# Optimization experiments

Measured on AMD Instinct MI355X. Metric: run time of the kernel, lower is better.

The kernel has to match this reference:

```python
import jax, jax.numpy as jnp
import numpy as np

BETA = 4.0  # temperature of soft cluster assignment in filling loss


def _pairwise_sq_dist(a, b):
    # a: [N,D], b: [K,D] -> [N,K] squared euclidean distances
    return (jnp.sum(a * a, -1, keepdims=True)
            - 2.0 * (a @ b.T)
            + jnp.sum(b * b, -1)[None, :])


def setup_inputs() -> dict:
    key = jax.random.key(0)
    k1, k2, k3, k4 = jax.random.split(key, 4)
    N, D, K = 131072, 64, 16
    x = jax.random.normal(k1, (N, D), jnp.float32)
    cluster_centers = jax.random.normal(k2, (K, D), jnp.float32)
    target = jax.random.normal(k3, (N, D), jnp.float32)
    ft = jax.random.uniform(k4, (K,), jnp.float32)
    filling_target = ft / ft.sum()
    # prediction = kmeans assignment of the fixed target set (computed once, constant)
    prediction = jnp.argmin(_pairwise_sq_dist(target, cluster_centers), axis=-1)
    return {"x": x, "cluster_centers": cluster_centers,
            "filling_target": filling_target, "target": target,
            "prediction": prediction}


def reference(x, cluster_centers, filling_target, target, prediction):
    N, D = x.shape
    Nt = target.shape[0]
    K = cluster_centers.shape[0]
    BIG = jnp.finfo(x.dtype).max  # padding value that sorts to the end

    d2 = _pairwise_sq_dist(x, cluster_centers)  # [N,K]

    # --- cluster filling MSE: soft assignment fractions vs filling_target ---
    soft = jax.nn.softmax(-BETA * d2, axis=-1)          # [N,K]
    filling = soft.mean(axis=0)                          # [K]
    loss_fil = jnp.mean((filling - filling_target) ** 2)

    # --- per-cluster sorted (per-dimension 1D) Wasserstein distance ---
    pred_x = jax.lax.stop_gradient(jnp.argmin(d2, axis=-1))  # kmeans_predict(x).detach()
    L = min(N, Nt)  # static upper bound on per-cluster min_size
    rows = jnp.arange(L)

    loss_med = jnp.zeros((), x.dtype)
    for k in range(K):  # fixed structural loop over clusters
        mx = pred_x == k
        mt = prediction == k
        m = jnp.minimum(mx.sum(), mt.sum())  # min_size (dynamic value, static shapes)
        # keep only the FIRST m members (original order), as x[in_cluster][:m]
        keep_x = mx & ((jnp.cumsum(mx) - 1) < m)
        keep_t = mt & ((jnp.cumsum(mt) - 1) < m)
        # mask out non-members with BIG so they sort to the bottom, sort per dim
        xs = jnp.sort(jnp.where(keep_x[:, None], x, BIG), axis=0)[:L]       # [L,D]
        ts = jnp.sort(jnp.where(keep_t[:, None], target, BIG), axis=0)[:L]  # [L,D]
        valid = (rows < m)[:, None]                                          # [L,1]
        diff = jnp.where(valid, jnp.abs(xs - ts), 0.0)
        # mean(|sort(x) - sort(y)|) over the m x D selected elements
        denom = (m * D).astype(x.dtype)
        loss_med = loss_med + jnp.where(m > 0, diff.sum() / denom, 0.0)

    return loss_fil + loss_med
```

## Files before the change

### kernel.cpp

```cpp
#include <hip/hip_runtime.h>
#include <stdint.h>

#define N_ROWS 131072
#define DIMS 64
#define KCL 16
#define BETA 4.0f
#define NBLK 512
#define CHUNK 16384
#define STH 1024
#define SEG_STRIDE 263168
#define VOFF (1u<<21)

typedef unsigned long long u64;
typedef unsigned int u32;

__device__ __forceinline__ u32 enc_f(float f) {
  u32 u = __float_as_uint(f);
  return (u & 0x80000000u) ? ~u : (u | 0x80000000u);
}
__device__ __forceinline__ float dec_f(u32 e) {
  u32 u = (e & 0x80000000u) ? (e & 0x7FFFFFFFu) : ~e;
  return __uint_as_float(u);
}
__device__ __forceinline__ u32 U4(u32 u) { return u ^ ((u >> 3) & 7u); }

#define CS(a,b,dd) { u32 _mn = min(a,b), _mx = max(a,b); a = (dd)?_mn:_mx; b = (dd)?_mx:_mn; }
#define CSV(A,B,D) { CS(A.x,B.x,D) CS(A.y,B.y,D) CS(A.z,B.z,D) CS(A.w,B.w,D) }

#define M16G(a,b,c,d,e,f,g,h,i2,j2,k2,l,m,n,o,p,D) \
  CS(a,i2,D) CS(b,j2,D) CS(c,k2,D) CS(d,l,D) CS(e,m,D) CS(f,n,D) CS(g,o,D) CS(h,p,D) \
  CS(a,e,D)  CS(b,f,D)  CS(c,g,D)  CS(d,h,D) CS(i2,m,D) CS(j2,n,D) CS(k2,o,D) CS(l,p,D) \
  CS(a,c,D)  CS(b,d,D)  CS(e,g,D)  CS(f,h,D) CS(i2,k2,D) CS(j2,l,D) CS(m,o,D) CS(n,p,D) \
  CS(a,b,D)  CS(c,d,D)  CS(e,f,D)  CS(g,h,D) CS(i2,j2,D) CS(k2,l,D) CS(m,n,D) CS(o,p,D)

#define SORT16G(a,b,c,d,e,f,g,h,i2,j2,k2,l,m,n,o,p,D) \
  CS(a,b,D) CS(c,d,!(D)) CS(e,f,D) CS(g,h,!(D)) CS(i2,j2,D) CS(k2,l,!(D)) CS(m,n,D) CS(o,p,!(D)) \
  CS(a,c,D) CS(b,d,D) CS(e,g,!(D)) CS(f,h,!(D)) CS(i2,k2,D) CS(j2,l,D) CS(m,o,!(D)) CS(n,p,!(D)) \
  CS(a,b,D) CS(c,d,D) CS(e,f,!(D)) CS(g,h,!(D)) CS(i2,j2,D) CS(k2,l,D) CS(m,n,!(D)) CS(o,p,!(D)) \
  CS(a,e,D) CS(b,f,D) CS(c,g,D) CS(d,h,D) CS(i2,m,!(D)) CS(j2,n,!(D)) CS(k2,o,!(D)) CS(l,p,!(D)) \
  CS(a,c,D) CS(b,d,D) CS(e,g,D) CS(f,h,D) CS(i2,k2,!(D)) CS(j2,l,!(D)) CS(m,o,!(D)) CS(n,p,!(D)) \
  CS(a,b,D) CS(c,d,D) CS(e,f,D) CS(g,h,D) CS(i2,j2,!(D)) CS(k2,l,!(D)) CS(m,n,!(D)) CS(o,p,!(D)) \
  M16G(a,b,c,d,e,f,g,h,i2,j2,k2,l,m,n,o,p,D)

#define MERGE16F(D) M16G(r0,r1,r2,r3,r4,r5,r6,r7,r8,r9,r10,r11,r12,r13,r14,r15,D)
#define SORT16F(D)  SORT16G(r0,r1,r2,r3,r4,r5,r6,r7,r8,r9,r10,r11,r12,r13,r14,r15,D)

#define LOADTILE16(src) \
  { uint4 _a0=src[U4(ub+0)],_a1=src[U4(ub+1)],_a2=src[U4(ub+2)],_a3=src[U4(ub+3)]; \
    r0=_a0.x;r1=_a0.y;r2=_a0.z;r3=_a0.w; r4=_a1.x;r5=_a1.y;r6=_a1.z;r7=_a1.w; \
    r8=_a2.x;r9=_a2.y;r10=_a2.z;r11=_a2.w; r12=_a3.x;r13=_a3.y;r14=_a3.z;r15=_a3.w; }

#define STORETILE16(dst) \
  { dst[U4(ub+0)]=make_uint4(r0,r1,r2,r3);   dst[U4(ub+1)]=make_uint4(r4,r5,r6,r7); \
    dst[U4(ub+2)]=make_uint4(r8,r9,r10,r11); dst[U4(ub+3)]=make_uint4(r12,r13,r14,r15); }

__device__ __forceinline__ void wave_tail(uint4* lds4, u32 RU, u32 Lw, u32 gbase,
                                          u32 k, u32 jtop, u32 lane)
{
  u32 j = jtop;
  while (j >= 32u) {
    u32 ud = j >> 3;
    if (lane < (Lw >> 4)) {
      u32 bu = RU + (((lane & ~(ud - 1u)) << 2) | (lane & (ud - 1u)));
      bool up = (((gbase + (bu << 2)) & k) == 0u);
      uint4 A0 = lds4[U4(bu)],           A1 = lds4[U4(bu + ud)],
            A2 = lds4[U4(bu + 2u * ud)], A3 = lds4[U4(bu + 3u * ud)];
      CSV(A0,A2,up) CSV(A1,A3,up)
      CSV(A0,A1,up) CSV(A2,A3,up)
      lds4[U4(bu)] = A0;           lds4[U4(bu + ud)] = A1;
      lds4[U4(bu + 2u * ud)] = A2; lds4[U4(bu + 3u * ud)] = A3;
    }
    j >>= 2;
  }
  if (j == 16u) {
    u32 total = Lw >> 3;
    for (u32 inst = lane; inst < total; inst += 64u) {
      u32 bu = RU + (((inst & ~3u) << 1) | (inst & 3u));
      bool up = (((gbase + (bu << 2)) & k) == 0u);
      uint4 A = lds4[U4(bu)], B = lds4[U4(bu + 4u)];
      CSV(A,B,up)
      lds4[U4(bu)] = A; lds4[U4(bu + 4u)] = B;
    }
  }
}

__device__ __forceinline__ void cross1(uint4* lds4, u32 Wn, u32 gb, u32 k, u32 jtop, u32 tid)
{
  u32 ud = jtop >> 2;
  u32 total = Wn >> 3;
  for (u32 inst = tid; inst < total; inst += STH) {
    u32 bu = ((inst & ~(ud - 1u)) << 1) | (inst & (ud - 1u));
    bool up = (((gb + (bu << 2)) & k) == 0u);
    uint4 A = lds4[U4(bu)], B = lds4[U4(bu + ud)];
    CSV(A,B,up)
    lds4[U4(bu)] = A; lds4[U4(bu + ud)] = B;
  }
}
__device__ __forceinline__ void cross2(uint4* lds4, u32 Wn, u32 gb, u32 k, u32 jtop, u32 tid)
{
  u32 ud = jtop >> 3;
  u32 total = Wn >> 4;
  for (u32 inst = tid; inst < total; inst += STH) {
    u32 bu = ((inst & ~(ud - 1u)) << 2) | (inst & (ud - 1u));
    bool up = (((gb + (bu << 2)) & k) == 0u);
    uint4 A0 = lds4[U4(bu)],            A1 = lds4[U4(bu + ud)],
          A2 = lds4[U4(bu + 2u * ud)],  A3 = lds4[U4(bu + 3u * ud)];
    CSV(A0,A2,up) CSV(A1,A3,up)
    CSV(A0,A1,up) CSV(A2,A3,up)
    lds4[U4(bu)] = A0;           lds4[U4(bu + ud)] = A1;
    lds4[U4(bu + 2u * ud)] = A2; lds4[U4(bu + 3u * ud)] = A3;
  }
}
__device__ __forceinline__ void cross3(uint4* lds4, u32 Wn, u32 gb, u32 k, u32 jtop, u32 tid)
{
  u32 ud = jtop >> 4;
  u32 total = Wn >> 5;
  for (u32 inst = tid; inst < total; inst += STH) {
    u32 bu = ((inst & ~(ud - 1u)) << 3) | (inst & (ud - 1u));
    bool up = (((gb + (bu << 2)) & k) == 0u);
    uint4 A0 = lds4[U4(bu)],            A1 = lds4[U4(bu + ud)],
          A2 = lds4[U4(bu + 2u * ud)],  A3 = lds4[U4(bu + 3u * ud)],
          A4 = lds4[U4(bu + 4u * ud)],  A5 = lds4[U4(bu + 5u * ud)],
          A6 = lds4[U4(bu + 6u * ud)],  A7 = lds4[U4(bu + 7u * ud)];
    CSV(A0,A4,up) CSV(A1,A5,up) CSV(A2,A6,up) CSV(A3,A7,up)
    CSV(A0,A2,up) CSV(A1,A3,up) CSV(A4,A6,up) CSV(A5,A7,up)
    CSV(A0,A1,up) CSV(A2,A3,up) CSV(A4,A5,up) CSV(A6,A7,up)
    lds4[U4(bu)] = A0;           lds4[U4(bu + ud)] = A1;
    lds4[U4(bu + 2u * ud)] = A2; lds4[U4(bu + 3u * ud)] = A3;
    lds4[U4(bu + 4u * ud)] = A4; lds4[U4(bu + 5u * ud)] = A5;
    lds4[U4(bu + 6u * ud)] = A6; lds4[U4(bu + 7u * ud)] = A7;
  }
}

__global__ __launch_bounds__(256) void k_assign(
    const float* __restrict__ x, const float* __restrict__ centers,
    const int* __restrict__ predT, int* __restrict__ predX,
    float* __restrict__ fill_sum, u32* __restrict__ histX, u32* __restrict__ histT)
{
  __shared__ float c[KCL][DIMS];
  __shared__ float cn[KCL];
  __shared__ float fs[KCL];
  __shared__ u32 hx[KCL], ht[KCL];
  int tid = threadIdx.x;
  for (int t = tid; t < KCL * DIMS; t += 256) c[t / DIMS][t % DIMS] = centers[t];
  if (tid < KCL) { fs[tid] = 0.f; hx[tid] = 0; ht[tid] = 0; }
  __syncthreads();
  if (tid < KCL) {
    float s = 0.f;
    for (int d = 0; d < DIMS; ++d) s += c[tid][d] * c[tid][d];
    cn[tid] = s;
  }
  __syncthreads();
  int i = blockIdx.x * 256 + tid;
  const float4* xr = (const float4*)(x + (size_t)i * DIMS);
  float dot[KCL];
#pragma unroll
  for (int k = 0; k < KCL; ++k) dot[k] = 0.f;
  for (int t = 0; t < DIMS / 4; ++t) {
    float4 v = xr[t];
#pragma unroll
    for (int k = 0; k < KCL; ++k)
      dot[k] += v.x * c[k][4 * t] + v.y * c[k][4 * t + 1] + v.z * c[k][4 * t + 2] + v.w * c[k][4 * t + 3];
  }
  float sc[KCL];
  float smin = 3.0e38f; int kmin = 0;
#pragma unroll
  for (int k = 0; k < KCL; ++k) {
    sc[k] = cn[k] - 2.f * dot[k];
    if (sc[k] < smin) { smin = sc[k]; kmin = k; }
  }
  float e[KCL]; float esum = 0.f;
#pragma unroll
  for (int k = 0; k < KCL; ++k) { e[k] = expf(-BETA * (sc[k] - smin)); esum += e[k]; }
  float inv = 1.f / esum;
#pragma unroll
  for (int k = 0; k < KCL; ++k) atomicAdd(&fs[k], e[k] * inv);
  predX[i] = kmin;
  atomicAdd(&hx[kmin], 1u);
  atomicAdd(&ht[predT[i]], 1u);
  __syncthreads();
  if (tid < KCL) {
    histX[blockIdx.x * KCL + tid] = hx[tid];
    histT[blockIdx.x * KCL + tid] = ht[tid];
    atomicAdd(&fill_sum[tid], fs[tid]);
  }
}

__global__ __launch_bounds__(512) void k_scan(
    const u32* __restrict__ histX, const u32* __restrict__ histT,
    u32* __restrict__ baseX, u32* __restrict__ baseT,
    const float* __restrict__ fill_sum, const float* __restrict__ ftarget,
    int* __restrict__ m_out, float* __restrict__ w_out,
    int* __restrict__ p_out, int* __restrict__ pOff_out, int* __restrict__ mOff_out,
    int* __restrict__ nlo_out, float* __restrict__ loss_fil)
{
  __shared__ u32 part[2][KCL][17];
  __shared__ u32 tot[2][KCL];
  __shared__ float sq[KCL];
  __shared__ int sp[KCL];
  __shared__ int smv[KCL];
  int tid = threadIdx.x;
  int side = tid >> 8;
  int rem = tid & 255;
  int c = rem >> 4;
  int sub = rem & 15;
  const u32* hist = side ? histT : histX;
  u32* base = side ? baseT : baseX;
  int b0 = sub * 32;
  u32 s = 0;
  for (int b = b0; b < b0 + 32; ++b) s += hist[b * KCL + c];
  part[side][c][sub] = s;
  __syncthreads();
  if (sub == 0) {
    u32 run = 0;
    for (int t = 0; t < 16; ++t) { u32 v = part[side][c][t]; part[side][c][t] = run; run += v; }
    tot[side][c] = run;
  }
  __syncthreads();
  u32 run = part[side][c][sub];
  for (int b = b0; b < b0 + 32; ++b) { base[b * KCL + c] = run; run += hist[b * KCL + c]; }
  if (tid < KCL) {
    int m = min((int)tot[0][tid], (int)tot[1][tid]);
    m_out[tid] = m;
    smv[tid] = m;
    w_out[tid] = (m > 0) ? 1.f / ((float)m * (float)DIMS) : 0.f;
    int pp = 32;
    while (pp < m) pp <<= 1;
    sp[tid] = pp;
    p_out[tid] = pp;
    int nlo = 0;
    if (pp > CHUNK) {
      int nch = pp / CHUNK;
      for (int j = 1; j < nch; j += 2) {
        int v = m - j * CHUNK;
        if (v < 0) v = 0;
        if (v > CHUNK) v = CHUNK;
        nlo += CHUNK - v;
      }
    }
    nlo_out[tid] = nlo;
    float d = fill_sum[tid] / (float)N_ROWS - ftarget[tid];
    sq[tid] = d * d;
  }
  __syncthreads();
  if (tid == 0) {
    float s2 = 0.f;
    int acc = 0, macc = 0;
    for (int k = 0; k < KCL; ++k) {
      s2 += sq[k];
      pOff_out[k] = acc;
      acc += sp[k];
      mOff_out[k] = macc;
      macc += smv[k];
    }
    pOff_out[KCL] = acc;
    mOff_out[KCL] = macc;
    *loss_fil = s2 / (float)KCL;
  }
}

__global__ __launch_bounds__(256) void k_rank(
    const int* __restrict__ predX, const int* __restrict__ predT,
    const u32* __restrict__ baseX, const u32* __restrict__ baseT,
    const int* __restrict__ mG, const int* __restrict__ mOffG,
    int* __restrict__ idxX, int* __restrict__ idxT)
{
  __shared__ int wcX[4][KCL], wcT[4][KCL];
  __shared__ int smo[KCL], sm2[KCL];
  int tid = threadIdx.x;
  int lane = tid & 63, wave = tid >> 6;
  if (tid < KCL) { smo[tid] = mOffG[tid]; sm2[tid] = mG[tid]; }
  int i = blockIdx.x * 256 + tid;
  int kx = predX[i], kt = predT[i];
  u64 below = (1ull << lane) - 1ull;
  int lrX = 0, lrT = 0;
  for (int cc = 0; cc < KCL; ++cc) {
    u64 mx = __ballot(kx == cc);
    u64 mt = __ballot(kt == cc);
    if (kx == cc) lrX = __popcll(mx & below);
    if (kt == cc) lrT = __popcll(mt & below);
    if (lane == 0) { wcX[wave][cc] = __popcll(mx); wcT[wave][cc] = __popcll(mt); }
  }
  __syncthreads();
  int wbX = 0, wbT = 0;
  for (int w2 = 0; w2 < wave; ++w2) { wbX += wcX[w2][kx]; wbT += wcT[w2][kt]; }
  int rX = (int)baseX[blockIdx.x * KCL + kx] + wbX + lrX;
  int rT = (int)baseT[blockIdx.x * KCL + kt] + wbT + lrT;
  if (rX < sm2[kx]) idxX[smo[kx] + rX] = i;
  if (rT < sm2[kt]) idxT[smo[kt] + rT] = i;
}

__global__ __launch_bounds__(256) void k_gather(
    const float* __restrict__ x, const float* __restrict__ tgt,
    const int* __restrict__ idxX, const int* __restrict__ idxT,
    const int* __restrict__ pOffG, const int* __restrict__ mOffG,
    const int* __restrict__ mG, const int* __restrict__ pG,
    u32* __restrict__ valX, u32* __restrict__ valT, int d0, int Dbc)
{
  __shared__ int spOff[KCL + 1];
  __shared__ int smo[KCL], sm2[KCL], sp2[KCL];
  __shared__ float pl[32][257];
  __shared__ int sRowX[256], sRowT[256];
  __shared__ u32 sPv[256];
  int tid = threadIdx.x;
  if (tid <= KCL) spOff[tid] = pOffG[tid];
  if (tid < KCL) { smo[tid] = mOffG[tid]; sm2[tid] = mG[tid]; sp2[tid] = pG[tid]; }
  __syncthreads();
  int pos = blockIdx.x * 256 + tid;
  bool inr = pos < spOff[KCL];
  int c = 0, rel = 0;
  bool vld = false;
  if (inr) {
#pragma unroll
    for (int cc = 1; cc < KCL; ++cc) c += (pos >= spOff[cc]) ? 1 : 0;
    rel = pos - spOff[c];
    vld = rel < sm2[c];
  }

  if (Dbc == 64) {
    int w = vld ? (smo[c] + rel) : 0;
    sRowX[tid] = vld ? idxX[w] : -1;
    sRowT[tid] = vld ? idxT[w] : -1;
    sPv[tid] = inr ? ((sp2[c] > CHUNK && ((rel >> 14) & 1)) ? 0u : 0xFFFFFFFFu) : 0u;
    __syncthreads();
#pragma unroll
    for (int side = 0; side < 2; ++side) {
      const float* src = side ? tgt : x;
      const int* sRow = side ? sRowT : sRowX;
      u32* dst = side ? valT : valX;
#pragma unroll
      for (int h = 0; h < 2; ++h) {
        int h0 = h * 32;
        for (int idx = tid; idx < 256 * 8; idx += 256) {
          int r = idx >> 3, f = idx & 7;
          int row = sRow[r];
          if (row >= 0) {
            float4 v = *(const float4*)(src + (size_t)row * DIMS + d0 + h0 + f * 4);
            pl[f * 4 + 0][r] = v.x;
            pl[f * 4 + 1][r] = v.y;
            pl[f * 4 + 2][r] = v.z;
            pl[f * 4 + 3][r] = v.w;
          }
        }
        __syncthreads();
        if (inr) {
          bool v2 = sRow[tid] >= 0;
          u32 pv = sPv[tid];
          for (int dl = 0; dl < 32; ++dl) {
            u32 e = v2 ? enc_f(pl[dl][tid]) : pv;
            dst[(size_t)(h0 + dl) * SEG_STRIDE + pos] = e;
          }
        }
        __syncthreads();
      }
    }
    return;
  }

  if (!inr) return;
  u32* dx = valX + pos;
  u32* dt = valT + pos;
  if (vld) {
    int w = smo[c] + rel;
    int iX = idxX[w], iT = idxT[w];
    const float* xr = x + (size_t)iX * DIMS + d0;
    const float* tr = tgt + (size_t)iT * DIMS + d0;
    for (int d = 0; d < Dbc; ++d) {
      dx[(size_t)d * SEG_STRIDE] = enc_f(xr[d]);
      dt[(size_t)d * SEG_STRIDE] = enc_f(tr[d]);
    }
  } else {
    u32 pv = (sp2[c] > CHUNK && ((rel >> 14) & 1)) ? 0u : 0xFFFFFFFFu;
    for (int d = 0; d < Dbc; ++d) {
      dx[(size_t)d * SEG_STRIDE] = pv;
      dt[(size_t)d * SEG_STRIDE] = pv;
    }
  }
}

__global__ __launch_bounds__(STH, 8) void k_sort(
    u32* __restrict__ vbase, const int* __restrict__ pG, const int* __restrict__ pOffG,
    const int* __restrict__ mG)
{
  __shared__ __align__(16) u32 lds[CHUNK];
  uint4* lds4 = (uint4*)lds;
  int t = blockIdx.x, c = -1, sub = 0, acc = 0;
  for (int cc = 0; cc < KCL; ++cc) {
    int pc0 = pG[cc];
    int nc = (pc0 > CHUNK) ? (pc0 / CHUNK) : 1;
    if (t < acc + nc) { c = cc; sub = t - acc; break; }
    acc += nc;
  }
  if (c < 0) return;
  int pc = pG[c];
  u32 CH = (u32)min(pc, CHUNK);
  u32 gb = (u32)sub * (u32)CHUNK;
  int v = mG[c] - (int)gb;
  if (v > (int)CH) v = (int)CH;
  if (v <= 0) return;
  u32 W = 32u;
  while (W < (u32)v) W <<= 1;
  if (W > CH) W = CH;
  bool desc = (pc > CHUNK) && (sub & 1);
  u32 inv = desc ? 0xFFFFFFFFu : 0u;
  u32* seg = vbase + (size_t)blockIdx.y * SEG_STRIDE + pOffG[c] + gb;
  uint4* gp4 = (uint4*)seg;
  u32 tid = threadIdx.x;
  u32 lane = tid & 63u;
  u32 wv = tid >> 6;
  u32 ub = tid << 2;
  u32 bas = tid << 4;
  bool act = (bas < W);
  u32 RU = wv << 8;
  u32 runBase = wv << 10;
  bool wact = (runBase < W);
  u32 Lw = W - runBase; if (Lw > 1024u) Lw = 1024u;
  u32 r0,r1,r2,r3,r4,r5,r6,r7,r8,r9,r10,r11,r12,r13,r14,r15;

  if (act) {
    uint4 a0 = gp4[ub + 0], a1 = gp4[ub + 1], a2 = gp4[ub + 2], a3 = gp4[ub + 3];
    r0 = a0.x^inv; r1 = a0.y^inv; r2  = a0.z^inv; r3  = a0.w^inv;
    r4 = a1.x^inv; r5 = a1.y^inv; r6  = a1.z^inv; r7  = a1.w^inv;
    r8 = a2.x^inv; r9 = a2.y^inv; r10 = a2.z^inv; r11 = a2.w^inv;
    r12 = a3.x^inv; r13 = a3.y^inv; r14 = a3.z^inv; r15 = a3.w^inv;
    bool D = ((bas & 16u) == 0u);
    SORT16F(D);
    STORETILE16(lds4);
  }
  if (wact) {
    for (u32 k = 32u; k <= Lw; k <<= 1) {
      wave_tail(lds4, RU, Lw, 0u, k, k >> 1, lane);
      if (act) {
        LOADTILE16(lds4);
        bool D = ((bas & k) == 0u);
        MERGE16F(D);
        STORETILE16(lds4);
      }
    }
  }

  if (W >= 2048u) {
    __syncthreads();
    for (u32 k = 2048u; k <= W; k <<= 1) {
      u32 jt = k >> 1;
      if (jt >= 8192u) {
        cross3(lds4, W, 0u, k, 8192u, tid);
        __syncthreads();
        cross1(lds4, W, 0u, k, 1024u, tid);
        __syncthreads();
      } else if (jt == 4096u) {
        cross3(lds4, W, 0u, k, 4096u, tid);
        __syncthreads();
      } else if (jt == 2048u) {
        cross2(lds4, W, 0u, k, 2048u, tid);
        __syncthreads();
      } else {
        cross1(lds4, W, 0u, k, 1024u, tid);
        __syncthreads();
      }
      if (wact) {
        wave_tail(lds4, RU, Lw, 0u, k, 512u, lane);
        if (act) {
          LOADTILE16(lds4);
          bool D = ((bas & k) == 0u);
          MERGE16F(D);
          STORETILE16(lds4);
        }
      }
      if (k < W) __syncthreads();
    }
  }

  __syncthreads();
  for (u32 uu = tid; (uu << 2) < W; uu += STH) {
    uint4 q = lds4[U4(uu)];
    q.x ^= inv; q.y ^= inv; q.z ^= inv; q.w ^= inv;
    gp4[uu] = q;
  }
}

__global__ __launch_bounds__(256) void k_gpass(
    u32* __restrict__ vbase, const int* __restrict__ pG, const int* __restrict__ pOffG,
    int kk, int j)
{
  u32* base = vbase + (size_t)blockIdx.y * SEG_STRIDE;
  int pb[KCL]; int tot = 0;
#pragma unroll
  for (int c = 0; c < KCL; ++c) {
    pb[c] = tot;
    int pc = pG[c];
    if (pc >= kk) tot += pc >> 1;
  }
  for (int g4 = (blockIdx.x * 256 + threadIdx.x) << 2; g4 < tot; g4 += gridDim.x * 256 * 4) {
    int c = 0;
#pragma unroll
    for (int cc = 1; cc < KCL; ++cc) c += (g4 >= pb[cc]) ? 1 : 0;
    int u = g4 - pb[c];
    int i = ((u & ~(j - 1)) << 1) | (u & (j - 1));
    bool up = ((i & kk) == 0);
    u32* s2 = base + pOffG[c];
    uint4 A = *(const uint4*)(s2 + i);
    uint4 B = *(const uint4*)(s2 + i + j);
    CS(A.x, B.x, up) CS(A.y, B.y, up) CS(A.z, B.z, up) CS(A.w, B.w, up)
    *(uint4*)(s2 + i) = A;
    *(uint4*)(s2 + i + j) = B;
  }
}

__global__ __launch_bounds__(STH) void k_gfinish(
    u32* __restrict__ vbase, const int* __restrict__ pG, const int* __restrict__ pOffG, int kk)
{
  __shared__ __align__(16) u32 lds[CHUNK];
  uint4* lds4 = (uint4*)lds;
  int t = blockIdx.x, c = -1, sub = 0, acc = 0;
  for (int cc = 0; cc < KCL; ++cc) {
    int pc = pG[cc];
    if (pc < kk) continue;
    int nc = pc / CHUNK;
    if (t < acc + nc) { c = cc; sub = t - acc; break; }
    acc += nc;
  }
  if (c < 0) return;
  u32 gb = (u32)sub * (u32)CHUNK;
  u32* seg = vbase + (size_t)blockIdx.y * SEG_STRIDE + pOffG[c] + gb;
  uint4* gp4 = (uint4*)seg;
  u32 tid = threadIdx.x;
  u32 lane = tid & 63u;
  u32 wv = tid >> 6;
  u32 RU = wv << 8;
  u32 ub = tid << 2;
  u32 bas = tid << 4;
  u32 r0,r1,r2,r3,r4,r5,r6,r7,r8,r9,r10,r11,r12,r13,r14,r15;

  for (u32 uu = tid; uu < CHUNK / 4; uu += STH) lds4[U4(uu)] = gp4[uu];
  __syncthreads();
  cross3(lds4, (u32)CHUNK, gb, (u32)kk, 8192u, tid);
  __syncthreads();
  cross1(lds4, (u32)CHUNK, gb, (u32)kk, 1024u, tid);
  __syncthreads();
  wave_tail(lds4, RU, 1024u, gb, (u32)kk, 512u, lane);
  {
    LOADTILE16(lds4);
    bool up = (((gb + bas) & (u32)kk) == 0u);
    MERGE16F(up);
    STORETILE16(lds4);
  }
  __syncthreads();
  for (u32 uu = tid; uu < CHUNK / 4; uu += STH) gp4[uu] = lds4[U4(uu)];
}

__global__ __launch_bounds__(256) void k_reduce(
    const u32* __restrict__ valX, const u32* __restrict__ valT,
    const int* __restrict__ pOffG, const int* __restrict__ mOffG,
    const int* __restrict__ nloG,
    const float* __restrict__ wG, float* __restrict__ lossAcc)
{
  __shared__ int spOff[KCL];
  __shared__ int smo[KCL + 1];
  __shared__ int snlo[KCL];
  __shared__ float swt[KCL];
  __shared__ float red[256];
  int tid = threadIdx.x;
  if (tid <= KCL) smo[tid] = mOffG[tid];
  if (tid < KCL) { spOff[tid] = pOffG[tid]; snlo[tid] = nloG[tid]; swt[tid] = wG[tid]; }
  __syncthreads();
  int d = blockIdx.y;
  const u32* vx = valX + (size_t)d * SEG_STRIDE;
  const u32* vt = valT + (size_t)d * SEG_STRIDE;
  int M = smo[KCL];
  float s = 0.f;
  for (int w = blockIdx.x * 256 + tid; w < M; w += gridDim.x * 256) {
    int c = 0;
#pragma unroll
    for (int cc = 1; cc < KCL; ++cc) c += (w >= smo[cc]) ? 1 : 0;
    int pos = spOff[c] + snlo[c] + (w - smo[c]);
    float a = dec_f(vx[pos]), b = dec_f(vt[pos]);
    s += fabsf(a - b) * swt[c];
  }
  red[tid] = s;
  __syncthreads();
  for (int st = 128; st > 0; st >>= 1) {
    if (tid < st) red[tid] += red[tid + st];
    __syncthreads();
  }
  if (tid == 0) atomicAdd(lossAcc, red[0]);
}

__global__ void k_final(const float* __restrict__ lossAcc, const float* __restrict__ loss_fil,
                        float* __restrict__ out)
{
  out[0] = *lossAcc + *loss_fil;
}

extern "C" void kernel_launch(void* const* d_in, const int* in_sizes, int n_in,
                              void* d_out, int out_size, void* d_ws, size_t ws_size,
                              hipStream_t stream)
{
  const float* x       = (const float*)d_in[0];
  const float* centers = (const float*)d_in[1];
  const float* ftarget = (const float*)d_in[2];
  const float* tgt     = (const float*)d_in[3];
  const int*   predT   = (const int*)d_in[4];
  float* out = (float*)d_out;

  char* ws = (char*)d_ws;
  float* fill_sum = (float*)(ws + 0);
  float* lossAcc  = (float*)(ws + 64);
  float* loss_fil = (float*)(ws + 68);
  int*   m_buf    = (int*)(ws + 128);
  float* w_buf    = (float*)(ws + 192);
  int*   p_buf    = (int*)(ws + 256);
  int*   pOff     = (int*)(ws + 320);
  int*   mOff     = (int*)(ws + 400);
  u32* histX = (u32*)(ws + 512);
  u32* histT = (u32*)(ws + 512 + 32768);
  u32* baseX = (u32*)(ws + 512 + 65536);
  u32* baseT = (u32*)(ws + 512 + 98304);
  int* predX = (int*)(ws + 131584);
  int* idxX  = (int*)(ws + 655872);
  int* idxT  = (int*)(ws + 1180160);
  int* nlo_buf = (int*)(ws + 1704448);
  u32* vbase = (u32*)(ws + VOFF);

  size_t avail_elems = (ws_size > VOFF) ? ((ws_size - VOFF) / 4) : 0;
  int Db = (int)(avail_elems / (2ull * SEG_STRIDE));
  if (Db > DIMS) Db = DIMS;
  if (Db >= 4) Db &= ~3;
  if (Db < 1) Db = 1;

  hipMemsetAsync(ws, 0, 128, stream);
  k_assign<<<NBLK, 256, 0, stream>>>(x, centers, predT, predX, fill_sum, histX, histT);
  k_scan<<<1, 512, 0, stream>>>(histX, histT, baseX, baseT, fill_sum, ftarget,
                                m_buf, w_buf, p_buf, pOff, mOff, nlo_buf, loss_fil);
  k_rank<<<NBLK, 256, 0, stream>>>(predX, predT, baseX, baseT, m_buf, mOff, idxX, idxT);

  for (int d0 = 0; d0 < DIMS; d0 += Db) {
    int Dbc = (Db < DIMS - d0) ? Db : (DIMS - d0);
    u32* valX = vbase;
    u32* valT = vbase + (size_t)Dbc * SEG_STRIDE;
    k_gather<<<1028, 256, 0, stream>>>(x, tgt, idxX, idxT, pOff, mOff, m_buf, p_buf,
                                       valX, valT, d0, Dbc);
    k_sort<<<dim3(28, 2 * Dbc), STH, 0, stream>>>(vbase, p_buf, pOff, m_buf);
    for (int kk = 2 * CHUNK; kk <= N_ROWS; kk <<= 1) {
      int gx = (kk == 2 * CHUNK) ? 32 : 8;
      for (int j = kk >> 1; j >= CHUNK; j >>= 1)
        k_gpass<<<dim3(gx, 2 * Dbc), 256, 0, stream>>>(vbase, p_buf, pOff, kk, j);
      k_gfinish<<<dim3(18, 2 * Dbc), STH, 0, stream>>>(vbase, p_buf, pOff, kk);
    }
    k_reduce<<<dim3(32, Dbc), 256, 0, stream>>>(valX, valT, pOff, mOff, nlo_buf,
                                                w_buf, lossAcc);
  }
  k_final<<<1, 1, 0, stream>>>(lossAcc, loss_fil, out);
}
```

Baseline: 599.3 us.

## Fuse small-cluster loss reduction into target sort kernel

The per-dimension sort is split into an X sort kernel and a T sort kernel. For clusters that fit in one chunk, the T sort kernel reads the already sorted X values and accumulates the weighted absolute difference directly, so those sorted T values are never written back to global memory. The separate reduce kernel now covers only the large multi-chunk clusters with fewer blocks. This saves a global write and re-read for small clusters, but it serialises the two sorts into back-to-back launches with half the blocks each, and it depends on the X sort finishing before the T sort reads its output.

```diff
diff --git a/kernel.cpp b/kernel.cpp
--- a/kernel.cpp
+++ b/kernel.cpp
@@ -378,7 +378,7 @@
   }
 }
 
-__global__ __launch_bounds__(STH, 8) void k_sort(
+__global__ __launch_bounds__(STH, 8) void k_sortX(
     u32* __restrict__ vbase, const int* __restrict__ pG, const int* __restrict__ pOffG,
     const int* __restrict__ mG)
 {
@@ -479,6 +479,149 @@
   }
 }
 
+__global__ __launch_bounds__(STH, 8) void k_sortT(
+    u32* __restrict__ vbase, const int* __restrict__ pG, const int* __restrict__ pOffG,
+    const int* __restrict__ mG, const float* __restrict__ wG,
+    float* __restrict__ lossAcc, int Dbc)
+{
+  __shared__ __align__(16) u32 lds[CHUNK];
+  uint4* lds4 = (uint4*)lds;
+  int t = blockIdx.x, c = -1, sub = 0, acc = 0;
+  for (int cc = 0; cc < KCL; ++cc) {
+    int pc0 = pG[cc];
+    int nc = (pc0 > CHUNK) ? (pc0 / CHUNK) : 1;
+    if (t < acc + nc) { c = cc; sub = t - acc; break; }
+    acc += nc;
+  }
+  if (c < 0) return;
+  int pc = pG[c];
+  u32 CH = (u32)min(pc, CHUNK);
+  u32 gb = (u32)sub * (u32)CHUNK;
+  int v = mG[c] - (int)gb;
+  if (v > (int)CH) v = (int)CH;
+  if (v <= 0) return;
+  u32 W = 32u;
+  while (W < (u32)v) W <<= 1;
+  if (W > CH) W = CH;
+  bool big = (pc > CHUNK);
+  bool desc = big && (sub & 1);
+  u32 inv = desc ? 0xFFFFFFFFu : 0u;
+  u32* segX = vbase + (size_t)blockIdx.y * SEG_STRIDE + pOffG[c] + gb;
+  u32* segT = segX + (size_t)Dbc * SEG_STRIDE;
+  uint4* gp4 = (uint4*)segT;
+  const uint4* gpX4 = (const uint4*)segX;
+  u32 tid = threadIdx.x;
+  u32 lane = tid & 63u;
+  u32 wv = tid >> 6;
+  u32 ub = tid << 2;
+  u32 bas = tid << 4;
+  bool act = (bas < W);
+  u32 RU = wv << 8;
+  u32 runBase = wv << 10;
+  bool wact = (runBase < W);
+  u32 Lw = W - runBase; if (Lw > 1024u) Lw = 1024u;
+  u32 r0,r1,r2,r3,r4,r5,r6,r7,r8,r9,r10,r11,r12,r13,r14,r15;
+
+  if (act) {
+    uint4 a0 = gp4[ub + 0], a1 = gp4[ub + 1], a2 = gp4[ub + 2], a3 = gp4[ub + 3];
+    r0 = a0.x^inv; r1 = a0.y^inv; r2  = a0.z^inv; r3  = a0.w^inv;
+    r4 = a1.x^inv; r5 = a1.y^inv; r6  = a1.z^inv; r7  = a1.w^inv;
+    r8 = a2.x^inv; r9 = a2.y^inv; r10 = a2.z^inv; r11 = a2.w^inv;
+    r12 = a3.x^inv; r13 = a3.y^inv; r14 = a3.z^inv; r15 = a3.w^inv;
+    bool D = ((bas & 16u) == 0u);
+    SORT16F(D);
+    STORETILE16(lds4);
+  }
+  if (wact) {
+    for (u32 k = 32u; k <= Lw; k <<= 1) {
+      wave_tail(lds4, RU, Lw, 0u, k, k >> 1, lane);
+      if (act) {
+        LOADTILE16(lds4);
+        bool D = ((bas & k) == 0u);
+        MERGE16F(D);
+        STORETILE16(lds4);
+      }
+    }
+  }
+
+  if (W >= 2048u) {
+    __syncthreads();
+    for (u32 k = 2048u; k <= W; k <<= 1) {
+      u32 jt = k >> 1;
+      if (jt >= 8192u) {
+        cross3(lds4, W, 0u, k, 8192u, tid);
+        __syncthreads();
+        cross1(lds4, W, 0u, k, 1024u, tid);
+        __syncthreads();
+      } else if (jt == 4096u) {
+        cross3(lds4, W, 0u, k, 4096u, tid);
+        __syncthreads();
+      } else if (jt == 2048u) {
+        cross2(lds4, W, 0u, k, 2048u, tid);
+        __syncthreads();
+      } else {
+        cross1(lds4, W, 0u, k, 1024u, tid);
+        __syncthreads();
+      }
+      if (wact) {
+        wave_tail(lds4, RU, Lw, 0u, k, 512u, lane);
+        if (act) {
+          LOADTILE16(lds4);
+          bool D = ((bas & k) == 0u);
+          MERGE16F(D);
+          STORETILE16(lds4);
+        }
+      }
+      if (k < W) __syncthreads();
+    }
+  }
+  __syncthreads();
+
+  if (big) {
+    for (u32 uu = tid; (uu << 2) < W; uu += STH) {
+      uint4 q = lds4[U4(uu)];
+      q.x ^= inv; q.y ^= inv; q.z ^= inv; q.w ^= inv;
+      gp4[uu] = q;
+    }
+    return;
+  }
+
+  float s = 0.f;
+  if (act) {
+    LOADTILE16(lds4);
+    uint4 b0 = gpX4[ub + 0], b1 = gpX4[ub + 1], b2 = gpX4[ub + 2], b3 = gpX4[ub + 3];
+    u32 vv = (u32)v;
+    if (bas + 0u  < vv) s += fabsf(dec_f(b0.x) - dec_f(r0));
+    if (bas + 1u  < vv) s += fabsf(dec_f(b0.y) - dec_f(r1));
+    if (bas + 2u  < vv) s += fabsf(dec_f(b0.z) - dec_f(r2));
+    if (bas + 3u  < vv) s += fabsf(dec_f(b0.w) - dec_f(r3));
+    if (bas + 4u  < vv) s += fabsf(dec_f(b1.x) - dec_f(r4));
+    if (bas + 5u  < vv) s += fabsf(dec_f(b1.y) - dec_f(r5));
+    if (bas + 6u  < vv) s += fabsf(dec_f(b1.z) - dec_f(r6));
+    if (bas + 7u  < vv) s += fabsf(dec_f(b1.w) - dec_f(r7));
+    if (bas + 8u  < vv) s += fabsf(dec_f(b2.x) - dec_f(r8));
+    if (bas + 9u  < vv) s += fabsf(dec_f(b2.y) - dec_f(r9));
+    if (bas + 10u < vv) s += fabsf(dec_f(b2.z) - dec_f(r10));
+    if (bas + 11u < vv) s += fabsf(dec_f(b2.w) - dec_f(r11));
+    if (bas + 12u < vv) s += fabsf(dec_f(b3.x) - dec_f(r12));
+    if (bas + 13u < vv) s += fabsf(dec_f(b3.y) - dec_f(r13));
+    if (bas + 14u < vv) s += fabsf(dec_f(b3.z) - dec_f(r14));
+    if (bas + 15u < vv) s += fabsf(dec_f(b3.w) - dec_f(r15));
+  }
+  s *= wG[c];
+  for (int o = 32; o > 0; o >>= 1) s += __shfl_down(s, o, 64);
+  __syncthreads();
+  float* lf = (float*)lds;
+  if (lane == 0) lf[wv] = s;
+  __syncthreads();
+  if (tid == 0) {
+    float tt = 0.f;
+#pragma unroll
+    for (int i2 = 0; i2 < STH / 64; ++i2) tt += lf[i2];
+    atomicAdd(lossAcc, tt);
+  }
+}
+
 __global__ __launch_bounds__(256) void k_gpass(
     u32* __restrict__ vbase, const int* __restrict__ pG, const int* __restrict__ pOffG,
     int kk, int j)
@@ -549,31 +692,35 @@
   for (u32 uu = tid; uu < CHUNK / 4; uu += STH) gp4[uu] = lds4[U4(uu)];
 }
 
-__global__ __launch_bounds__(256) void k_reduce(
+__global__ __launch_bounds__(256) void k_reduce_big(
     const u32* __restrict__ valX, const u32* __restrict__ valT,
-    const int* __restrict__ pOffG, const int* __restrict__ mOffG,
-    const int* __restrict__ nloG,
+    const int* __restrict__ pOffG, const int* __restrict__ mG,
+    const int* __restrict__ pG, const int* __restrict__ nloG,
     const float* __restrict__ wG, float* __restrict__ lossAcc)
 {
+  __shared__ int bnd[KCL + 1];
   __shared__ int spOff[KCL];
-  __shared__ int smo[KCL + 1];
   __shared__ int snlo[KCL];
   __shared__ float swt[KCL];
   __shared__ float red[256];
   int tid = threadIdx.x;
-  if (tid <= KCL) smo[tid] = mOffG[tid];
+  if (tid == 0) {
+    int mb = 0;
+    for (int k = 0; k < KCL; ++k) { bnd[k] = mb; if (pG[k] > CHUNK) mb += mG[k]; }
+    bnd[KCL] = mb;
+  }
   if (tid < KCL) { spOff[tid] = pOffG[tid]; snlo[tid] = nloG[tid]; swt[tid] = wG[tid]; }
   __syncthreads();
+  int M = bnd[KCL];
   int d = blockIdx.y;
   const u32* vx = valX + (size_t)d * SEG_STRIDE;
   const u32* vt = valT + (size_t)d * SEG_STRIDE;
-  int M = smo[KCL];
   float s = 0.f;
   for (int w = blockIdx.x * 256 + tid; w < M; w += gridDim.x * 256) {
     int c = 0;
 #pragma unroll
-    for (int cc = 1; cc < KCL; ++cc) c += (w >= smo[cc]) ? 1 : 0;
-    int pos = spOff[c] + snlo[c] + (w - smo[c]);
+    for (int cc = 1; cc < KCL; ++cc) c += (w >= bnd[cc]) ? 1 : 0;
+    int pos = spOff[c] + snlo[c] + (w - bnd[c]);
     float a = dec_f(vx[pos]), b = dec_f(vt[pos]);
     s += fabsf(a - b) * swt[c];
   }
@@ -583,7 +730,7 @@
     if (tid < st) red[tid] += red[tid + st];
     __syncthreads();
   }
-  if (tid == 0) atomicAdd(lossAcc, red[0]);
+  if (tid == 0 && red[0] != 0.f) atomicAdd(lossAcc, red[0]);
 }
 
 __global__ void k_final(const float* __restrict__ lossAcc, const float* __restrict__ loss_fil,
@@ -640,15 +787,17 @@
     u32* valT = vbase + (size_t)Dbc * SEG_STRIDE;
     k_gather<<<1028, 256, 0, stream>>>(x, tgt, idxX, idxT, pOff, mOff, m_buf, p_buf,
                                        valX, valT, d0, Dbc);
-    k_sort<<<dim3(28, 2 * Dbc), STH, 0, stream>>>(vbase, p_buf, pOff, m_buf);
+    k_sortX<<<dim3(28, Dbc), STH, 0, stream>>>(vbase, p_buf, pOff, m_buf);
+    k_sortT<<<dim3(28, Dbc), STH, 0, stream>>>(vbase, p_buf, pOff, m_buf,
+                                               w_buf, lossAcc, Dbc);
     for (int kk = 2 * CHUNK; kk <= N_ROWS; kk <<= 1) {
       int gx = (kk == 2 * CHUNK) ? 32 : 8;
       for (int j = kk >> 1; j >= CHUNK; j >>= 1)
         k_gpass<<<dim3(gx, 2 * Dbc), 256, 0, stream>>>(vbase, p_buf, pOff, kk, j);
       k_gfinish<<<dim3(18, 2 * Dbc), STH, 0, stream>>>(vbase, p_buf, pOff, kk);
     }
-    k_reduce<<<dim3(32, Dbc), 256, 0, stream>>>(valX, valT, pOff, mOff, nlo_buf,
-                                                w_buf, lossAcc);
+    k_reduce_big<<<dim3(8, Dbc), 256, 0, stream>>>(valX, valT, pOff, m_buf, p_buf,
+                                                   nlo_buf, w_buf, lossAcc);
   }
   k_final<<<1, 1, 0, stream>>>(lossAcc, loss_fil, out);
 }
```

New measurement: 621.6 us. +3.7%, slower.

## Split single-chunk cluster sort into full and partial halves to skip padding work

Applied to the files above, without the earlier changes.

For clusters whose padded size equals exactly one chunk, the sort kernel now sorts the lower half (always full) and the partially filled upper half as independent bitonic sequences. The upper half is sorted in the opposite direction over only its occupied power-of-two width, and its padding is set to 0 so it lands in the correct place. The two halves are then combined with a final merge step. This avoids running full-chunk bitonic stages over mostly padding elements, at the cost of extra branching, more barriers, and a more intricate index scheme.

```diff
diff --git a/kernel.cpp b/kernel.cpp
--- a/kernel.cpp
+++ b/kernel.cpp
@@ -118,6 +118,57 @@
   for (u32 inst = tid; inst < total; inst += STH) {
     u32 bu = ((inst & ~(ud - 1u)) << 3) | (inst & (ud - 1u));
     bool up = (((gb + (bu << 2)) & k) == 0u);
+    uint4 A0 = lds4[U4(bu)],            A1 = lds4[U4(bu + ud)],
+          A2 = lds4[U4(bu + 2u * ud)],  A3 = lds4[U4(bu + 3u * ud)],
+          A4 = lds4[U4(bu + 4u * ud)],  A5 = lds4[U4(bu + 5u * ud)],
+          A6 = lds4[U4(bu + 6u * ud)],  A7 = lds4[U4(bu + 7u * ud)];
+    CSV(A0,A4,up) CSV(A1,A5,up) CSV(A2,A6,up) CSV(A3,A7,up)
+    CSV(A0,A2,up) CSV(A1,A3,up) CSV(A4,A6,up) CSV(A5,A7,up)
+    CSV(A0,A1,up) CSV(A2,A3,up) CSV(A4,A5,up) CSV(A6,A7,up)
+    lds4[U4(bu)] = A0;           lds4[U4(bu + ud)] = A1;
+    lds4[U4(bu + 2u * ud)] = A2; lds4[U4(bu + 3u * ud)] = A3;
+    lds4[U4(bu + 4u * ud)] = A4; lds4[U4(bu + 5u * ud)] = A5;
+    lds4[U4(bu + 6u * ud)] = A6; lds4[U4(bu + 7u * ud)] = A7;
+  }
+}
+
+__device__ __forceinline__ void crossB1(uint4* lds4, u32 Wn, u32 k, u32 jtop, u32 tid)
+{
+  u32 ud = jtop >> 2;
+  u32 total = Wn >> 3;
+  for (u32 inst = tid; inst < total; inst += STH) {
+    u32 buL = ((inst & ~(ud - 1u)) << 1) | (inst & (ud - 1u));
+    bool up = (((buL << 2) & k) == 0u);
+    u32 bu = buL + 2048u;
+    uint4 A = lds4[U4(bu)], B = lds4[U4(bu + ud)];
+    CSV(A,B,up)
+    lds4[U4(bu)] = A; lds4[U4(bu + ud)] = B;
+  }
+}
+__device__ __forceinline__ void crossB2(uint4* lds4, u32 Wn, u32 k, u32 jtop, u32 tid)
+{
+  u32 ud = jtop >> 3;
+  u32 total = Wn >> 4;
+  for (u32 inst = tid; inst < total; inst += STH) {
+    u32 buL = ((inst & ~(ud - 1u)) << 2) | (inst & (ud - 1u));
+    bool up = (((buL << 2) & k) == 0u);
+    u32 bu = buL + 2048u;
+    uint4 A0 = lds4[U4(bu)],            A1 = lds4[U4(bu + ud)],
+          A2 = lds4[U4(bu + 2u * ud)],  A3 = lds4[U4(bu + 3u * ud)];
+    CSV(A0,A2,up) CSV(A1,A3,up)
+    CSV(A0,A1,up) CSV(A2,A3,up)
+    lds4[U4(bu)] = A0;           lds4[U4(bu + ud)] = A1;
+    lds4[U4(bu + 2u * ud)] = A2; lds4[U4(bu + 3u * ud)] = A3;
+  }
+}
+__device__ __forceinline__ void crossB3(uint4* lds4, u32 Wn, u32 k, u32 jtop, u32 tid)
+{
+  u32 ud = jtop >> 4;
+  u32 total = Wn >> 5;
+  for (u32 inst = tid; inst < total; inst += STH) {
+    u32 buL = ((inst & ~(ud - 1u)) << 3) | (inst & (ud - 1u));
+    bool up = (((buL << 2) & k) == 0u);
+    u32 bu = buL + 2048u;
     uint4 A0 = lds4[U4(bu)],            A1 = lds4[U4(bu + ud)],
           A2 = lds4[U4(bu + 2u * ud)],  A3 = lds4[U4(bu + 3u * ud)],
           A4 = lds4[U4(bu + 4u * ud)],  A5 = lds4[U4(bu + 5u * ud)],
@@ -237,6 +288,8 @@
         if (v > CHUNK) v = CHUNK;
         nlo += CHUNK - v;
       }
+    } else if (pp == CHUNK) {
+      nlo = CHUNK - m;
     }
     nlo_out[tid] = nlo;
     float d = fill_sum[tid] / (float)N_ROWS - ftarget[tid];
@@ -321,7 +374,13 @@
     int w = vld ? (smo[c] + rel) : 0;
     sRowX[tid] = vld ? idxX[w] : -1;
     sRowT[tid] = vld ? idxT[w] : -1;
-    sPv[tid] = inr ? ((sp2[c] > CHUNK && ((rel >> 14) & 1)) ? 0u : 0xFFFFFFFFu) : 0u;
+    u32 pv = 0u;
+    if (inr) {
+      if (sp2[c] > CHUNK)       pv = ((rel >> 14) & 1) ? 0u : 0xFFFFFFFFu;
+      else if (sp2[c] == CHUNK) pv = 0u;
+      else                      pv = 0xFFFFFFFFu;
+    }
+    sPv[tid] = pv;
     __syncthreads();
 #pragma unroll
     for (int side = 0; side < 2; ++side) {
@@ -345,9 +404,9 @@
         __syncthreads();
         if (inr) {
           bool v2 = sRow[tid] >= 0;
-          u32 pv = sPv[tid];
+          u32 pvv = sPv[tid];
           for (int dl = 0; dl < 32; ++dl) {
-            u32 e = v2 ? enc_f(pl[dl][tid]) : pv;
+            u32 e = v2 ? enc_f(pl[dl][tid]) : pvv;
             dst[(size_t)(h0 + dl) * SEG_STRIDE + pos] = e;
           }
         }
@@ -370,7 +429,10 @@
       dt[(size_t)d * SEG_STRIDE] = enc_f(tr[d]);
     }
   } else {
-    u32 pv = (sp2[c] > CHUNK && ((rel >> 14) & 1)) ? 0u : 0xFFFFFFFFu;
+    u32 pv;
+    if (sp2[c] > CHUNK)       pv = ((rel >> 14) & 1) ? 0u : 0xFFFFFFFFu;
+    else if (sp2[c] == CHUNK) pv = 0u;
+    else                      pv = 0xFFFFFFFFu;
     for (int d = 0; d < Dbc; ++d) {
       dx[(size_t)d * SEG_STRIDE] = pv;
       dt[(size_t)d * SEG_STRIDE] = pv;
@@ -398,9 +460,18 @@
   int v = mG[c] - (int)gb;
   if (v > (int)CH) v = (int)CH;
   if (v <= 0) return;
-  u32 W = 32u;
-  while (W < (u32)v) W <<= 1;
-  if (W > CH) W = CH;
+  bool dual = (pc == CHUNK);
+  u32 W, WB = 0;
+  if (dual) {
+    W = (u32)CHUNK;
+    u32 vt = (u32)v - 8192u;
+    WB = 32u;
+    while (WB < vt) WB <<= 1;
+  } else {
+    W = 32u;
+    while (W < (u32)v) W <<= 1;
+    if (W > CH) W = CH;
+  }
   bool desc = (pc > CHUNK) && (sub & 1);
   u32 inv = desc ? 0xFFFFFFFFu : 0u;
   u32* seg = vbase + (size_t)blockIdx.y * SEG_STRIDE + pOffG[c] + gb;
@@ -410,57 +481,98 @@
   u32 wv = tid >> 6;
   u32 ub = tid << 2;
   u32 bas = tid << 4;
-  bool act = (bas < W);
   u32 RU = wv << 8;
-  u32 runBase = wv << 10;
-  bool wact = (runBase < W);
-  u32 Lw = W - runBase; if (Lw > 1024u) Lw = 1024u;
+  u32 subBase = 0, IV = inv, Wl = W;
+  if (dual) {
+    if (wv < 8u) { subBase = 0u;    IV = 0u;          Wl = 8192u; }
+    else         { subBase = 8192u; IV = 0xFFFFFFFFu; Wl = WB;    }
+  }
+  u32 el = bas - subBase;
+  bool act = el < Wl;
+  u32 runL = (wv << 10) - subBase;
+  bool wact = runL < Wl;
+  u32 Lw = Wl - runL; if (Lw > 1024u) Lw = 1024u;
+  u32 gAdj = 0u - subBase;
   u32 r0,r1,r2,r3,r4,r5,r6,r7,r8,r9,r10,r11,r12,r13,r14,r15;
 
   if (act) {
     uint4 a0 = gp4[ub + 0], a1 = gp4[ub + 1], a2 = gp4[ub + 2], a3 = gp4[ub + 3];
-    r0 = a0.x^inv; r1 = a0.y^inv; r2  = a0.z^inv; r3  = a0.w^inv;
-    r4 = a1.x^inv; r5 = a1.y^inv; r6  = a1.z^inv; r7  = a1.w^inv;
-    r8 = a2.x^inv; r9 = a2.y^inv; r10 = a2.z^inv; r11 = a2.w^inv;
-    r12 = a3.x^inv; r13 = a3.y^inv; r14 = a3.z^inv; r15 = a3.w^inv;
-    bool D = ((bas & 16u) == 0u);
+    r0 = a0.x^IV; r1 = a0.y^IV; r2  = a0.z^IV; r3  = a0.w^IV;
+    r4 = a1.x^IV; r5 = a1.y^IV; r6  = a1.z^IV; r7  = a1.w^IV;
+    r8 = a2.x^IV; r9 = a2.y^IV; r10 = a2.z^IV; r11 = a2.w^IV;
+    r12 = a3.x^IV; r13 = a3.y^IV; r14 = a3.z^IV; r15 = a3.w^IV;
+    bool D = ((el & 16u) == 0u);
     SORT16F(D);
     STORETILE16(lds4);
+  } else if (dual) {
+    r0=0;r1=0;r2=0;r3=0;r4=0;r5=0;r6=0;r7=0;r8=0;r9=0;r10=0;r11=0;r12=0;r13=0;r14=0;r15=0;
+    STORETILE16(lds4);
   }
   if (wact) {
     for (u32 k = 32u; k <= Lw; k <<= 1) {
-      wave_tail(lds4, RU, Lw, 0u, k, k >> 1, lane);
+      wave_tail(lds4, RU, Lw, gAdj, k, k >> 1, lane);
       if (act) {
         LOADTILE16(lds4);
-        bool D = ((bas & k) == 0u);
+        bool D = ((el & k) == 0u);
         MERGE16F(D);
         STORETILE16(lds4);
       }
     }
+  }
+
+  if (dual && WB >= 2048u) {
+    __syncthreads();
+    for (u32 k = 2048u; k <= WB; k <<= 1) {
+      u32 jt = k >> 1;
+      if (jt == 4096u) crossB3(lds4, WB, k, 4096u, tid);
+      else if (jt == 2048u) crossB2(lds4, WB, k, 2048u, tid);
+      else crossB1(lds4, WB, k, 1024u, tid);
+      __syncthreads();
+      if (wv >= 8u && wact) {
+        wave_tail(lds4, RU, Lw, gAdj, k, 512u, lane);
+        if (act) {
+          LOADTILE16(lds4);
+          bool D = ((el & k) == 0u);
+          MERGE16F(D);
+          STORETILE16(lds4);
+        }
+      }
+      __syncthreads();
+    }
+  }
+  if (dual && wv >= 8u && act) {
+    LOADTILE16(lds4);
+    r0^=IV; r1^=IV; r2^=IV; r3^=IV; r4^=IV; r5^=IV; r6^=IV; r7^=IV;
+    r8^=IV; r9^=IV; r10^=IV; r11^=IV; r12^=IV; r13^=IV; r14^=IV; r15^=IV;
+    STORETILE16(lds4);
   }
 
   if (W >= 2048u) {
     __syncthreads();
     for (u32 k = 2048u; k <= W; k <<= 1) {
       u32 jt = k >> 1;
+      u32 Wc = dual ? ((k == (u32)CHUNK) ? (u32)CHUNK : 8192u) : W;
       if (jt >= 8192u) {
-        cross3(lds4, W, 0u, k, 8192u, tid);
+        cross3(lds4, Wc, 0u, k, 8192u, tid);
         __syncthreads();
-        cross1(lds4, W, 0u, k, 1024u, tid);
+        cross1(lds4, Wc, 0u, k, 1024u, tid);
         __syncthreads();
       } else if (jt == 4096u) {
-        cross3(lds4, W, 0u, k, 4096u, tid);
+        cross3(lds4, Wc, 0u, k, 4096u, tid);
         __syncthreads();
       } else if (jt == 2048u) {
-        cross2(lds4, W, 0u, k, 2048u, tid);
+        cross2(lds4, Wc, 0u, k, 2048u, tid);
         __syncthreads();
       } else {
-        cross1(lds4, W, 0u, k, 1024u, tid);
+        cross1(lds4, Wc, 0u, k, 1024u, tid);
         __syncthreads();
       }
-      if (wact) {
-        wave_tail(lds4, RU, Lw, 0u, k, 512u, lane);
-        if (act) {
+      bool part = dual ? ((k == (u32)CHUNK) ? true : (wv < 8u)) : wact;
+      u32 LwT = dual ? 1024u : Lw;
+      if (part) {
+        wave_tail(lds4, RU, LwT, 0u, k, 512u, lane);
+        bool mact = dual ? ((k == (u32)CHUNK) ? true : (bas < 8192u)) : act;
+        if (mact) {
           LOADTILE16(lds4);
           bool D = ((bas & k) == 0u);
           MERGE16F(D);
```

New measurement: 611.6 us. +2.1%, slower.
